# Optimization experiments

Measured on AMD Instinct MI355X. Metric: run time of the kernel, lower is better.

The kernel has to match this reference:

```python
import jax, jax.numpy as jnp
import numpy as np

B, T = 64, 512
V, F, H = 30000, 256, 256
K = 32          # type_num
PAD, START, END = 0, 30, 31


def make_transition():
    # replicate the exact init order of the torch code
    t = jnp.zeros((K, K), jnp.float32)
    t = t.at[:, START].set(-10000.0)
    t = t.at[END, :].set(-10000.0)
    t = t.at[:, PAD].set(-10000.0)
    t = t.at[PAD, PAD].set(0.0)
    t = t.at[PAD, :END].set(0.0)
    return t


def setup_inputs() -> dict:
    key = jax.random.key(0)
    ks = jax.random.split(key, 12)
    x = jax.random.randint(ks[0], (B, T), 0, V, dtype=jnp.int32)
    tags = jax.random.randint(ks[1], (B, T), 1, START, dtype=jnp.int32)  # real tags, no pad/start/end
    lengths = jax.random.randint(ks[2], (B,), T // 2, T + 1, dtype=jnp.int32)
    mask = (jnp.arange(T, dtype=jnp.int32)[None, :] < lengths[:, None]).astype(jnp.int32)
    s = 0.05
    emb = jax.random.normal(ks[3], (V, F), jnp.float32) * (2.0 / (V + F)) ** 0.5 * 10  # xavier-ish
    w_ih_f = jax.random.normal(ks[4], (4 * H, F), jnp.float32) * s
    w_hh_f = jax.random.normal(ks[5], (4 * H, H), jnp.float32) * s
    b_f = jax.random.normal(ks[6], (4 * H,), jnp.float32) * s  # = b_ih + b_hh (they only ever sum)
    w_ih_b = jax.random.normal(ks[7], (4 * H, F), jnp.float32) * s
    w_hh_b = jax.random.normal(ks[8], (4 * H, H), jnp.float32) * s
    b_b = jax.random.normal(ks[9], (4 * H,), jnp.float32) * s
    w_fc = jax.random.normal(ks[10], (K, 2 * H), jnp.float32) * s
    b_fc = jax.random.normal(ks[11], (K,), jnp.float32) * s
    transition = make_transition()
    return dict(x=x, tags=tags, mask=mask, emb=emb,
                w_ih_f=w_ih_f, w_hh_f=w_hh_f, b_f=b_f,
                w_ih_b=w_ih_b, w_hh_b=w_hh_b, b_b=b_b,
                w_fc=w_fc, b_fc=b_fc, transition=transition)


def _lstm_scan(gx, w_hh):
    # gx: [T, B, 4H] precomputed input gates; PyTorch gate order i, f, g, o
    h0 = jnp.zeros((gx.shape[1], w_hh.shape[1]), gx.dtype)

    def step(carry, g):
        h, c = carry
        z = g + h @ w_hh.T
        i, f, gg, o = jnp.split(z, 4, axis=-1)
        c = jax.nn.sigmoid(f) * c + jax.nn.sigmoid(i) * jnp.tanh(gg)
        h = jax.nn.sigmoid(o) * jnp.tanh(c)
        return (h, c), h

    _, hs = jax.lax.scan(step, (h0, h0), gx)
    return hs  # [T, B, H]


def _crf_loss(scores, tags, mask, transition):
    # scores: [B, T, K], tags/mask: [B, T]
    maskf = mask.astype(scores.dtype)
    b_idx = jnp.arange(scores.shape[0])

    # ---- true path score ----
    first = transition[START, tags[:, 0]] + scores[b_idx, 0, tags[:, 0]]
    tag_sc = jnp.take_along_axis(scores, tags[..., None].astype(jnp.int32), axis=2)[..., 0]  # [B,T]
    tran_sc = transition[tags[:, :-1], tags[:, 1:]]  # [B,T-1]
    body = jnp.sum((tran_sc + tag_sc[:, 1:]) * maskf[:, 1:], axis=1)
    last_idx = jnp.sum(mask, axis=1) - 1
    last_tag = jnp.take_along_axis(tags, last_idx[:, None], axis=1)[:, 0]
    true_prob = first + body + transition[last_tag, END]

    # ---- partition (forward algorithm) via scan ----
    alpha0 = transition[START][None, :] + scores[:, 0]  # [B,K]

    def step(alpha, inp):
        sc, m = inp  # sc: [B,K], m: [B]
        new = jax.nn.logsumexp(alpha[:, :, None] + transition[None, :, :] + sc[:, None, :], axis=1)
        alpha = jnp.where(m[:, None] > 0, new, alpha)
        return alpha, None

    alpha, _ = jax.lax.scan(step, alpha0,
                            (scores.transpose(1, 0, 2)[1:], mask.T[1:]))
    total_prob = jax.nn.logsumexp(alpha + transition[:, END][None, :], axis=1)
    return -jnp.sum(true_prob - total_prob)


def reference(x, tags, mask, emb, w_ih_f, w_hh_f, b_f, w_ih_b, w_hh_b, b_b, w_fc, b_fc, transition):
    e = emb[x]                       # [B,T,F] embedding lookup (dropout = identity, eval mode)
    xt = e.transpose(1, 0, 2)        # [T,B,F]
    # forward direction
    h_f = _lstm_scan(xt @ w_ih_f.T + b_f, w_hh_f)           # [T,B,H]
    # backward direction: reverse time, scan, reverse back
    h_b = _lstm_scan((xt @ w_ih_b.T + b_b)[::-1], w_hh_b)[::-1]
    h = jnp.concatenate([h_f, h_b], axis=-1).transpose(1, 0, 2)  # [B,T,2H]
    scores = h @ w_fc.T + b_fc       # [B,T,K]
    return _crf_loss(scores, tags, mask, transition)
```

## Files before the change

### kernel.cpp

```cpp
#include <hip/hip_runtime.h>

typedef __attribute__((ext_vector_type(8))) short short8;
typedef __attribute__((ext_vector_type(4))) float floatx4;
typedef __attribute__((ext_vector_type(8))) int int8v;

__device__ __forceinline__ float bf2f(unsigned short u) {
    union { unsigned int i; float f; } c; c.i = ((unsigned int)u) << 16; return c.f;
}
__device__ __forceinline__ float asf(unsigned int u) {
    union { unsigned int i; float f; } c; c.i = u; return c.f;
}
__device__ __forceinline__ unsigned short f2bf(float f) {
    union { float f; unsigned int i; } c; c.f = f;
    unsigned int u = c.i;
    return (unsigned short)((u + 0x7FFFu + ((u >> 16) & 1u)) >> 16);
}
__device__ __forceinline__ unsigned short f2bf_rz(float f) {
    union { float f; unsigned int i; } c; c.f = f;
    return (unsigned short)(c.i >> 16);
}
__device__ __forceinline__ float sigm(float x) {
    return __builtin_amdgcn_rcpf(1.f + __expf(-x));
}
__device__ __forceinline__ float tanh_(float x) {
    return 1.f - 2.f * __builtin_amdgcn_rcpf(1.f + __expf(2.f * x));
}

__device__ __forceinline__ void glds16(const void* g, void* l) {
    __builtin_amdgcn_global_load_lds((const __attribute__((address_space(1))) unsigned int*)g,
                                     (__attribute__((address_space(3))) unsigned int*)l, 16, 0, 0);
}

__global__ void k_prep(const int* __restrict__ x, const float* __restrict__ emb,
                       unsigned short* __restrict__ et,
                       const float* __restrict__ wihf, const float* __restrict__ wihb,
                       const float* __restrict__ wfc, unsigned short* __restrict__ wbf,
                       const float* __restrict__ whhf, const float* __restrict__ whhb,
                       unsigned char* __restrict__ w8) {
    const int bid = blockIdx.x;
    if (bid < 4096) {
        int id = bid * 256 + threadIdx.x;
        int m = id >> 5, fi = (id & 31) << 3;
        int b = m & 63, t = m >> 6;
        int v = x[b * 512 + t];
        const float4* s = (const float4*)(emb + ((size_t)v << 8) + fi);
        float4 a = s[0], q = s[1];
        uint4 o;
        o.x = (unsigned)f2bf(a.x) | ((unsigned)f2bf(a.y) << 16);
        o.y = (unsigned)f2bf(a.z) | ((unsigned)f2bf(a.w) << 16);
        o.z = (unsigned)f2bf(q.x) | ((unsigned)f2bf(q.y) << 16);
        o.w = (unsigned)f2bf(q.z) | ((unsigned)f2bf(q.w) << 16);
        *(uint4*)(et + ((size_t)m << 8) + fi) = o;
    } else if (bid < 6176) {
        int i = (bid - 4096) * 256 + threadIdx.x;
        if (i >= 532480) return;
        float v;
        if (i < 524288) {
            int r = (i >> 8) & 1023, c = i & 255;
            int src = (256 * (r & 3) + (r >> 2)) * 256 + c;
            v = (i < 262144) ? wihf[src] : wihb[src];
        } else {
            v = wfc[i - 524288];
        }
        wbf[i] = f2bf(v);
    } else {
        int i = (bid - 6176) * 256 + threadIdx.x;
        if (i >= 262144) return;
        int e = i * 2;
        float a = (e < 262144) ? whhf[e] : whhb[e - 262144];
        float b = (e + 1 < 262144) ? whhf[e + 1] : whhb[e + 1 - 262144];
        int p = __builtin_amdgcn_cvt_pk_fp8_f32(a, b, 0, false);
        *(unsigned short*)(w8 + e) = (unsigned short)(p & 0xffff);
    }
}

__global__ __launch_bounds__(256, 2) void k_gx(const unsigned short* __restrict__ et,
                                               const unsigned short* __restrict__ wcat,
                                               const float* __restrict__ bfv, const float* __restrict__ bbv,
                                               unsigned short* __restrict__ gx) {
    __shared__ unsigned short S[17408];
    unsigned short* As = S;
    unsigned short* Bs = S + 4096;
    const int tid = threadIdx.x;
    const int w = tid >> 6, l = tid & 63, quad = l >> 4, col = l & 15;
    const size_t m0 = (size_t)blockIdx.x * 128, n0 = (size_t)blockIdx.y * 128;
    floatx4 C[4][4];
    #pragma unroll
    for (int i = 0; i < 4; ++i)
        #pragma unroll
        for (int j = 0; j < 4; ++j) C[i][j] = (floatx4){0.f, 0.f, 0.f, 0.f};
    const int srow = tid >> 2, scol = (tid & 3) * 16;
    for (int it = 0; it < 8; ++it) {
        const char* ga = (const char*)et + (m0 + srow) * 512 + it * 64 + scol;
        const char* gb = (const char*)wcat + (n0 + srow) * 512 + it * 64 + scol;
        glds16(ga,             (char*)As + w * 1024);
        glds16(ga + 64 * 512,  (char*)As + 4096 + w * 1024);
        glds16(gb,             (char*)Bs + w * 1024);
        glds16(gb + 64 * 512,  (char*)Bs + 4096 + w * 1024);
        __syncthreads();
        short8 Af[4], Bf[4];
        #pragma unroll
        for (int i = 0; i < 4; ++i) {
            Af[i] = *(const short8*)(As + (((w & 1) * 64 + i * 16 + col) * 32 + quad * 8));
            Bf[i] = *(const short8*)(Bs + (((w >> 1) * 64 + i * 16 + col) * 32 + quad * 8));
        }
        #pragma unroll
        for (int i = 0; i < 4; ++i)
            #pragma unroll
            for (int j = 0; j < 4; ++j)
                C[i][j] = __builtin_amdgcn_mfma_f32_16x16x32_bf16(Af[i], Bf[j], C[i][j], 0, 0, 0);
        __syncthreads();
    }
    const int mw = (w & 1) * 64, nw = (w >> 1) * 64;
    #pragma unroll
    for (int j = 0; j < 4; ++j) {
        int nl_ = nw + j * 16 + col;
        int n = (int)n0 + nl_;
        int nl = n & 1023;
        int bidx = ((nl >> 2) & 255) + 256 * (nl & 3);
        float bias = (n < 1024) ? bfv[bidx] : bbv[bidx];
        #pragma unroll
        for (int i = 0; i < 4; ++i)
            #pragma unroll
            for (int r = 0; r < 4; ++r) {
                int ml = mw + i * 16 + quad * 4 + r;
                S[ml * 136 + nl_] = f2bf(C[i][j][r] + bias);
            }
    }
    __syncthreads();
    const int row_ = tid >> 4, seg = (tid & 15) * 8;
    const size_t gbase = (size_t)(n0 >> 10) * 33554432 + (size_t)(n0 & 1023);
    #pragma unroll
    for (int k = 0; k < 8; ++k) {
        int ml = k * 16 + row_;
        *(short8*)(gx + gbase + (m0 + ml) * 1024 + seg) = *(const short8*)(&S[ml * 136 + seg]);
    }
}

__global__ __launch_bounds__(512, 2) void k_lstm(const unsigned char* __restrict__ w8_all,
                                                 const unsigned short* __restrict__ gx_all,
                                                 unsigned short* __restrict__ hcat) {
    const int d = blockIdx.x >> 5, bg = blockIdx.x & 31;
    const int tid = threadIdx.x, w = tid >> 6, l = tid & 63, quad = l >> 4, col = l & 15;
    const unsigned char* W = w8_all + (size_t)d * 262144;
    const unsigned short* G = gx_all + (size_t)d * 33554432;
    __shared__ __align__(16) unsigned char hld[2][2][288];

    int8v Wb[4][2][2];
    #pragma unroll
    for (int g = 0; g < 4; ++g)
        #pragma unroll
        for (int nt = 0; nt < 2; ++nt)
            #pragma unroll
            for (int kt = 0; kt < 2; ++kt)
                Wb[g][nt][kt] = *(const int8v*)(W + (size_t)(256 * g + 32 * w + 16 * nt + col) * 256
                                                + kt * 128 + quad * 32);
    for (int i = tid; i < 288; i += 512) ((unsigned int*)hld)[i] = 0;

    const int b = l >> 5, u = 32 * w + (l & 31);
    const int bglob = 2 * bg + b;
    const int nts = quad & 1;
    const int hsel = (l >> 3) & 1;
    float cst = 0.f;
    const long gstep = d ? -65536 : 65536;
    const long hstep = d ? -32768 : 32768;
    const unsigned short* gp = G + ((size_t)((d ? 511 : 0) * 64 + bglob) * 1024 + u * 4);
    unsigned short* hp = hcat + ((size_t)((d ? 511 : 0) * 64 + bglob) * 512 + d * 256 + u);
    uint2 gq = *(const uint2*)gp;
    gp += gstep;
    __syncthreads();

    #pragma clang loop unroll(disable)
    for (int step = 0; step < 512; ++step) {
        const int cur = step & 1;
        int8v Af[2];
        #pragma unroll
        for (int kt = 0; kt < 2; ++kt)
            Af[kt] = *(const int8v*)(&hld[cur][hsel][kt * 128 + quad * 32]);
        float z[4];
        #pragma unroll
        for (int g = 0; g < 4; ++g) {
            floatx4 c0 = (floatx4){0.f, 0.f, 0.f, 0.f};
            floatx4 c1 = (floatx4){0.f, 0.f, 0.f, 0.f};
            #pragma unroll
            for (int kt = 0; kt < 2; ++kt) {
                c0 = __builtin_amdgcn_mfma_scale_f32_16x16x128_f8f6f4(
                    Af[kt], Wb[g][0][kt], c0, 0, 0, 0, 0x7f7f7f7f, 0, 0x7f7f7f7f);
                c1 = __builtin_amdgcn_mfma_scale_f32_16x16x128_f8f6f4(
                    Af[kt], Wb[g][1][kt], c1, 0, 0, 0, 0x7f7f7f7f, 0, 0x7f7f7f7f);
            }
            z[g] = nts ? c1[0] : c0[0];
        }
        float vi = z[0] + asf(gq.x << 16);
        float vf = z[1] + asf(gq.x & 0xffff0000u);
        float vg = z[2] + asf(gq.y << 16);
        float vo = z[3] + asf(gq.y & 0xffff0000u);
        gq = *(const uint2*)gp;
        gp += gstep;
        float cc = sigm(vf) * cst + sigm(vi) * tanh_(vg);
        cst = cc;
        float hf = sigm(vo) * tanh_(cc);
        *hp = f2bf_rz(hf);
        hp += hstep;
        int pk = __builtin_amdgcn_cvt_pk_fp8_f32(hf, hf, 0, false);
        hld[cur ^ 1][b][u] = (unsigned char)(pk & 0xff);
        __builtin_amdgcn_sched_barrier(0);
        asm volatile("s_waitcnt lgkmcnt(0)");
        __builtin_amdgcn_sched_barrier(0);
        __builtin_amdgcn_s_barrier();
        __builtin_amdgcn_sched_barrier(0);
    }
}

__global__ __launch_bounds__(256, 4) void k_scores(const unsigned short* __restrict__ hcat,
                                                   const unsigned short* __restrict__ wfc,
                                                   const float* __restrict__ bfc,
                                                   float* __restrict__ sc) {
    const int tid = threadIdx.x, w = tid >> 6, l = tid & 63, quad = l >> 4, col = l & 15;
    const int m0 = blockIdx.x * 64 + w * 16;
    floatx4 C0 = (floatx4){0.f, 0.f, 0.f, 0.f}, C1 = C0;
    #pragma unroll
    for (int kt = 0; kt < 16; ++kt) {
        short8 A  = *(const short8*)(hcat + (size_t)(m0 + col) * 512 + kt * 32 + quad * 8);
        short8 B0 = *(const short8*)(wfc + (size_t)col * 512 + kt * 32 + quad * 8);
        short8 B1 = *(const short8*)(wfc + (size_t)(16 + col) * 512 + kt * 32 + quad * 8);
        C0 = __builtin_amdgcn_mfma_f32_16x16x32_bf16(A, B0, C0, 0, 0, 0);
        C1 = __builtin_amdgcn_mfma_f32_16x16x32_bf16(A, B1, C1, 0, 0, 0);
    }
    float b0 = bfc[col], b1 = bfc[16 + col];
    #pragma unroll
    for (int r = 0; r < 4; ++r) {
        int m = m0 + quad * 4 + r;
        sc[(size_t)m * 32 + col] = C0[r] + b0;
        sc[(size_t)m * 32 + 16 + col] = C1[r] + b1;
    }
}

__global__ __launch_bounds__(1024, 1) void k_crf(const float* __restrict__ sc, const int* __restrict__ tags,
                                                 const int* __restrict__ mask, const float* __restrict__ tr,
                                                 float* __restrict__ out) {
    extern __shared__ __align__(16) char smem[];
    float* scl = (float*)smem;
    float* Tm  = scl + 16384;
    float* al  = Tm + 1056;
    int*   msk = (int*)(al + 64);
    const int b = blockIdx.x, tid = threadIdx.x;
    #pragma unroll
    for (int p = 0; p < 4; ++p) {
        int t = p * 128 + (tid >> 3), seg = (tid & 7) * 4;
        *(float4*)&scl[t * 32 + seg] = *(const float4*)&sc[((size_t)(t * 64 + b)) * 32 + seg];
    }
    if (tid < 512) msk[tid] = mask[b * 512 + tid];
    { int i = tid >> 5, j = tid & 31; Tm[i * 33 + j] = tr[tid]; }
    __syncthreads();
    float trueb = 0.f;
    if (tid < 64) {
        float acc = 0.f; int cnt = 0;
        for (int t = tid; t < 512; t += 64) cnt += msk[t];
        for (int t = tid + 1; t < 512; t += 64) {
            if (msk[t]) {
                int tg = tags[b * 512 + t], tp = tags[b * 512 + t - 1];
                acc += Tm[tp * 33 + tg] + scl[t * 32 + tg];
            }
        }
        #pragma unroll
        for (int m = 1; m < 64; m <<= 1) { acc += __shfl_xor(acc, m); cnt += __shfl_xor(cnt, m); }
        if (tid == 0) {
            int tg0 = tags[b * 512];
            float first = Tm[30 * 33 + tg0] + scl[tg0];
            int lt = tags[b * 512 + cnt - 1];
            trueb = first + acc + Tm[lt * 33 + 31];
        }
    }
    if (tid < 32) al[tid] = Tm[30 * 33 + tid] + scl[tid];
    __syncthreads();
    const int j = tid >> 5, i = tid & 31;
    int cur = 0;
    #pragma clang loop unroll(disable)
    for (int t = 1; t < 512; ++t) {
        float v = al[cur * 32 + i] + Tm[i * 33 + j];
        float mx = v;
        #pragma unroll
        for (int m = 1; m < 32; m <<= 1) mx = fmaxf(mx, __shfl_xor(mx, m));
        float e = __expf(v - mx);
        #pragma unroll
        for (int m = 1; m < 32; m <<= 1) e += __shfl_xor(e, m);
        float nv = mx + __logf(e) + scl[t * 32 + j];
        if (i == 0) al[(cur ^ 1) * 32 + j] = msk[t] ? nv : al[cur * 32 + j];
        __syncthreads();
        cur ^= 1;
    }
    if (tid < 32) {
        float v = al[cur * 32 + tid] + Tm[tid * 33 + 31];
        float mx = v;
        #pragma unroll
        for (int m = 1; m < 32; m <<= 1) mx = fmaxf(mx, __shfl_xor(mx, m));
        float e = __expf(v - mx);
        #pragma unroll
        for (int m = 1; m < 32; m <<= 1) e += __shfl_xor(e, m);
        if (tid == 0) atomicAdd(out, mx + __logf(e) - trueb);
    }
}

extern "C" void kernel_launch(void* const* d_in, const int* in_sizes, int n_in,
                              void* d_out, int out_size, void* d_ws, size_t ws_size,
                              hipStream_t stream) {
    const int* x      = (const int*)d_in[0];
    const int* tags   = (const int*)d_in[1];
    const int* mask   = (const int*)d_in[2];
    const float* emb  = (const float*)d_in[3];
    const float* wihf = (const float*)d_in[4];
    const float* whhf = (const float*)d_in[5];
    const float* bf_  = (const float*)d_in[6];
    const float* wihb = (const float*)d_in[7];
    const float* whhb = (const float*)d_in[8];
    const float* bb_  = (const float*)d_in[9];
    const float* wfc  = (const float*)d_in[10];
    const float* bfc  = (const float*)d_in[11];
    const float* tr   = (const float*)d_in[12];

    char* ws = (char*)d_ws;
    unsigned short* et   = (unsigned short*)(ws);
    unsigned short* wbf  = (unsigned short*)(ws + 16777216);
    unsigned char*  w8   = (unsigned char*)(ws + 17842176);
    unsigned short* gx   = (unsigned short*)(ws + 18366464);
    unsigned short* hcat = (unsigned short*)(ws + 152584192);
    float* sc            = (float*)(ws + 186138624);

    static bool attr_set = false;
    if (!attr_set) {
        hipFuncSetAttribute((const void*)k_crf, hipFuncAttributeMaxDynamicSharedMemorySize, 72064);
        attr_set = true;
    }

    hipMemsetAsync(d_out, 0, sizeof(float), stream);
    k_prep<<<7200, 256, 0, stream>>>(x, emb, et, wihf, wihb, wfc, wbf, whhf, whhb, w8);
    dim3 g2(256, 16);
    k_gx<<<g2, 256, 0, stream>>>(et, wbf, bf_, bb_, gx);
    k_lstm<<<64, 512, 0, stream>>>(w8, gx, hcat);
    k_scores<<<512, 256, 0, stream>>>(hcat, wbf + 524288, bfc, sc);
    k_crf<<<64, 1024, 72064, stream>>>(sc, tags, mask, tr, (float*)d_out);
}
```

Before: 853.5 us.

## Interleave two batch groups per LSTM block to hide recurrence latency

Each k_lstm block now processes two independent batch groups (A and B) in the same time loop, with separate hidden-state LDS buffers, cell states and gx/h pointers, and the grid is halved to 32 blocks. The MFMAs and gate nonlinearities of the two groups can overlap, hiding the per-step latency chain of the recurrence and sharing one barrier per step across both groups. In exchange, each block does twice the serial work per step and uses fewer CUs, so the per-step time may grow if the loop was not purely latency-bound.

New measurement: 1.155 ms. +35.4%, slower.

```diff
diff --git a/kernel.cpp b/kernel.cpp
--- a/kernel.cpp
+++ b/kernel.cpp
@@ -140,11 +140,11 @@
 __global__ __launch_bounds__(512, 2) void k_lstm(const unsigned char* __restrict__ w8_all,
                                                  const unsigned short* __restrict__ gx_all,
                                                  unsigned short* __restrict__ hcat) {
-    const int d = blockIdx.x >> 5, bg = blockIdx.x & 31;
+    const int d = blockIdx.x >> 4, bgA = blockIdx.x & 15, bgB = bgA + 16;
     const int tid = threadIdx.x, w = tid >> 6, l = tid & 63, quad = l >> 4, col = l & 15;
     const unsigned char* W = w8_all + (size_t)d * 262144;
     const unsigned short* G = gx_all + (size_t)d * 33554432;
-    __shared__ __align__(16) unsigned char hld[2][2][288];
+    __shared__ __align__(16) unsigned char hld[2][2][2][288];
 
     int8v Wb[4][2][2];
     #pragma unroll
@@ -155,29 +155,31 @@
             for (int kt = 0; kt < 2; ++kt)
                 Wb[g][nt][kt] = *(const int8v*)(W + (size_t)(256 * g + 32 * w + 16 * nt + col) * 256
                                                 + kt * 128 + quad * 32);
-    for (int i = tid; i < 288; i += 512) ((unsigned int*)hld)[i] = 0;
+    for (int i = tid; i < 576; i += 512) ((unsigned int*)hld)[i] = 0;
 
     const int b = l >> 5, u = 32 * w + (l & 31);
-    const int bglob = 2 * bg + b;
+    const int bglobA = 2 * bgA + b, bglobB = 2 * bgB + b;
     const int nts = quad & 1;
     const int hsel = (l >> 3) & 1;
-    float cst = 0.f;
+    float cstA = 0.f, cstB = 0.f;
     const long gstep = d ? -65536 : 65536;
     const long hstep = d ? -32768 : 32768;
-    const unsigned short* gp = G + ((size_t)((d ? 511 : 0) * 64 + bglob) * 1024 + u * 4);
-    unsigned short* hp = hcat + ((size_t)((d ? 511 : 0) * 64 + bglob) * 512 + d * 256 + u);
-    uint2 gq = *(const uint2*)gp;
-    gp += gstep;
+    const unsigned short* gpA = G + ((size_t)((d ? 511 : 0) * 64 + bglobA) * 1024 + u * 4);
+    const unsigned short* gpB = G + ((size_t)((d ? 511 : 0) * 64 + bglobB) * 1024 + u * 4);
+    unsigned short* hpA = hcat + ((size_t)((d ? 511 : 0) * 64 + bglobA) * 512 + d * 256 + u);
+    unsigned short* hpB = hcat + ((size_t)((d ? 511 : 0) * 64 + bglobB) * 512 + d * 256 + u);
+    uint2 gqA = *(const uint2*)gpA; gpA += gstep;
+    uint2 gqB = *(const uint2*)gpB; gpB += gstep;
     __syncthreads();
 
     #pragma clang loop unroll(disable)
     for (int step = 0; step < 512; ++step) {
         const int cur = step & 1;
-        int8v Af[2];
+        int8v AfA[2];
         #pragma unroll
         for (int kt = 0; kt < 2; ++kt)
-            Af[kt] = *(const int8v*)(&hld[cur][hsel][kt * 128 + quad * 32]);
-        float z[4];
+            AfA[kt] = *(const int8v*)(&hld[0][cur][hsel][kt * 128 + quad * 32]);
+        float zA[4];
         #pragma unroll
         for (int g = 0; g < 4; ++g) {
             floatx4 c0 = (floatx4){0.f, 0.f, 0.f, 0.f};
@@ -185,25 +187,60 @@
             #pragma unroll
             for (int kt = 0; kt < 2; ++kt) {
                 c0 = __builtin_amdgcn_mfma_scale_f32_16x16x128_f8f6f4(
-                    Af[kt], Wb[g][0][kt], c0, 0, 0, 0, 0x7f7f7f7f, 0, 0x7f7f7f7f);
+                    AfA[kt], Wb[g][0][kt], c0, 0, 0, 0, 0x7f7f7f7f, 0, 0x7f7f7f7f);
                 c1 = __builtin_amdgcn_mfma_scale_f32_16x16x128_f8f6f4(
-                    Af[kt], Wb[g][1][kt], c1, 0, 0, 0, 0x7f7f7f7f, 0, 0x7f7f7f7f);
+                    AfA[kt], Wb[g][1][kt], c1, 0, 0, 0, 0x7f7f7f7f, 0, 0x7f7f7f7f);
             }
-            z[g] = nts ? c1[0] : c0[0];
-        }
-        float vi = z[0] + asf(gq.x << 16);
-        float vf = z[1] + asf(gq.x & 0xffff0000u);
-        float vg = z[2] + asf(gq.y << 16);
-        float vo = z[3] + asf(gq.y & 0xffff0000u);
-        gq = *(const uint2*)gp;
-        gp += gstep;
-        float cc = sigm(vf) * cst + sigm(vi) * tanh_(vg);
-        cst = cc;
-        float hf = sigm(vo) * tanh_(cc);
-        *hp = f2bf_rz(hf);
-        hp += hstep;
-        int pk = __builtin_amdgcn_cvt_pk_fp8_f32(hf, hf, 0, false);
-        hld[cur ^ 1][b][u] = (unsigned char)(pk & 0xff);
+            zA[g] = nts ? c1[0] : c0[0];
+        }
+        int8v AfB[2];
+        #pragma unroll
+        for (int kt = 0; kt < 2; ++kt)
+            AfB[kt] = *(const int8v*)(&hld[1][cur][hsel][kt * 128 + quad * 32]);
+        float zB[4];
+        #pragma unroll
+        for (int g = 0; g < 4; ++g) {
+            floatx4 c0 = (floatx4){0.f, 0.f, 0.f, 0.f};
+            floatx4 c1 = (floatx4){0.f, 0.f, 0.f, 0.f};
+            #pragma unroll
+            for (int kt = 0; kt < 2; ++kt) {
+                c0 = __builtin_amdgcn_mfma_scale_f32_16x16x128_f8f6f4(
+                    AfB[kt], Wb[g][0][kt], c0, 0, 0, 0, 0x7f7f7f7f, 0, 0x7f7f7f7f);
+                c1 = __builtin_amdgcn_mfma_scale_f32_16x16x128_f8f6f4(
+                    AfB[kt], Wb[g][1][kt], c1, 0, 0, 0, 0x7f7f7f7f, 0, 0x7f7f7f7f);
+            }
+            zB[g] = nts ? c1[0] : c0[0];
+        }
+        {
+            float vi = zA[0] + asf(gqA.x << 16);
+            float vf = zA[1] + asf(gqA.x & 0xffff0000u);
+            float vg = zA[2] + asf(gqA.y << 16);
+            float vo = zA[3] + asf(gqA.y & 0xffff0000u);
+            gqA = *(const uint2*)gpA;
+            gpA += gstep;
+            float cc = sigm(vf) * cstA + sigm(vi) * tanh_(vg);
+            cstA = cc;
+            float hf = sigm(vo) * tanh_(cc);
+            *hpA = f2bf_rz(hf);
+            hpA += hstep;
+            int pk = __builtin_amdgcn_cvt_pk_fp8_f32(hf, hf, 0, false);
+            hld[0][cur ^ 1][b][u] = (unsigned char)(pk & 0xff);
+        }
+        {
+            float vi = zB[0] + asf(gqB.x << 16);
+            float vf = zB[1] + asf(gqB.x & 0xffff0000u);
+            float vg = zB[2] + asf(gqB.y << 16);
+            float vo = zB[3] + asf(gqB.y & 0xffff0000u);
+            gqB = *(const uint2*)gpB;
+            gpB += gstep;
+            float cc = sigm(vf) * cstB + sigm(vi) * tanh_(vg);
+            cstB = cc;
+            float hf = sigm(vo) * tanh_(cc);
+            *hpB = f2bf_rz(hf);
+            hpB += hstep;
+            int pk = __builtin_amdgcn_cvt_pk_fp8_f32(hf, hf, 0, false);
+            hld[1][cur ^ 1][b][u] = (unsigned char)(pk & 0xff);
+        }
         __builtin_amdgcn_sched_barrier(0);
         asm volatile("s_waitcnt lgkmcnt(0)");
         __builtin_amdgcn_sched_barrier(0);
@@ -337,7 +374,7 @@
     k_prep<<<7200, 256, 0, stream>>>(x, emb, et, wihf, wihb, wfc, wbf, whhf, whhb, w8);
     dim3 g2(256, 16);
     k_gx<<<g2, 256, 0, stream>>>(et, wbf, bf_, bb_, gx);
-    k_lstm<<<64, 512, 0, stream>>>(w8, gx, hcat);
+    k_lstm<<<32, 512, 0, stream>>>(w8, gx, hcat);
     k_scores<<<512, 256, 0, stream>>>(hcat, wbf + 524288, bfc, sc);
     k_crf<<<64, 1024, 72064, stream>>>(sc, tags, mask, tr, (float*)d_out);
 }
```
